# Kernel tuning notes

Hardware: AMD Instinct MI355X
Metric: run time of the kernel (lower is better)

Reference implementation:

```python
import jax, jax.numpy as jnp
import numpy as np

B, T, MAX_ITEMS = 128, 50, 32
NUM_PRODUCT, E, EW = 100000, 128, 16
D = E + EW  # rnn input/hidden size


def setup_inputs() -> dict:
    key = jax.random.key(0)
    ks = jax.random.split(key, 10)
    # items: 0 is padding; keep roughly half the slots padded (ragged baskets)
    items = jax.random.randint(ks[0], (B, T, MAX_ITEMS), 1, NUM_PRODUCT)
    keep = jax.random.uniform(ks[1], (B, T, MAX_ITEMS)) < 0.5
    keep = keep.at[:, :, 0].set(True)  # at least one item per basket
    items = jnp.where(keep, items, 0)
    flag = jax.random.randint(ks[2], (B, T, 1), 0, 2)
    x = jnp.concatenate([items, flag], axis=-1)  # [B,T,MAX_ITEMS+1], last col = flag
    lengths = jnp.full((B,), T, dtype=jnp.int64)
    hidden = jnp.zeros((1, B, D), dtype=jnp.float32)
    s_e = 1.0 / np.sqrt(E)
    s_d = 1.0 / np.sqrt(D)
    encode_w = jax.random.uniform(ks[3], (NUM_PRODUCT, E), minval=-0.1, maxval=0.1)
    encode_w = encode_w.at[0].set(0.0)  # padding_idx=0
    wchange_w = jax.random.normal(ks[4], (2, EW)) * 0.1
    wchange_w = wchange_w.at[0].set(0.0)  # padding_idx=0
    w_ih = jax.random.uniform(ks[5], (3 * D, D), minval=-s_d, maxval=s_d)
    w_hh = jax.random.uniform(ks[6], (3 * D, D), minval=-s_d, maxval=s_d)
    b_ih = jax.random.uniform(ks[7], (3 * D,), minval=-s_d, maxval=s_d)
    b_hh = jax.random.uniform(ks[8], (3 * D,), minval=-s_d, maxval=s_d)
    fc_w = jax.random.uniform(ks[9], (E, D), minval=-s_d, maxval=s_d)
    fc_b = jnp.zeros((E,), dtype=jnp.float32)
    return {"x": x, "lengths": lengths, "hidden": hidden,
            "encode_w": encode_w, "wchange_w": wchange_w,
            "w_ih": w_ih, "w_hh": w_hh, "b_ih": b_ih, "b_hh": b_hh,
            "fc_w": fc_w, "fc_b": fc_b}


def _embed_baskets(x, encode_w, wchange_w):
    items = x[..., :-1]                      # [B,T,I] product ids, 0 = pad
    flag = x[..., -1]                        # [B,T] 0/1 weight-change flag
    emb = encode_w[items]                    # [B,T,I,E] fused ragged gather
    mask = (items != 0).astype(emb.dtype)[..., None]
    cnt = jnp.maximum(mask.sum(axis=2), 1.0)
    pooled = (emb * mask).sum(axis=2) / cnt  # avg pool over real items [B,T,E]
    w = wchange_w[flag]                      # [B,T,EW]
    return jnp.concatenate([pooled, w], axis=-1)  # [B,T,D]


def _gru(seq, h0, w_ih, w_hh, b_ih, b_hh):
    # seq: [B,T,D], h0: [B,D]; torch GRU cell math
    def step(h, x_t):
        gi = x_t @ w_ih.T + b_ih             # [B,3D]
        gh = h @ w_hh.T + b_hh
        i_r, i_z, i_n = jnp.split(gi, 3, axis=-1)
        h_r, h_z, h_n = jnp.split(gh, 3, axis=-1)
        r = jax.nn.sigmoid(i_r + h_r)
        z = jax.nn.sigmoid(i_z + h_z)
        n = jnp.tanh(i_n + r * h_n)
        h_new = (1.0 - z) * n + z * h
        return h_new, h_new
    h_last, outs = jax.lax.scan(step, h0, jnp.swapaxes(seq, 0, 1))
    return jnp.swapaxes(outs, 0, 1), h_last  # [B,T,D], [B,D]


def reference(x, lengths, hidden, encode_w, wchange_w, w_ih, w_hh, b_ih, b_hh, fc_w, fc_b):
    seq = _embed_baskets(x, encode_w, wchange_w)         # [B,T,D]
    out, h_last = _gru(seq, hidden[0], w_ih, w_hh, b_ih, b_hh)
    dynamic_user = out @ fc_w.T + fc_b                   # [B,T,E]
    return dynamic_user, h_last[None]                    # h_u: [1,B,D]
```

## Files before the change

### kernel.cpp

```cpp
#include <hip/hip_runtime.h>
#include <math.h>

#define B_   128
#define T_   50
#define MI_  32
#define E_   128
#define EW_  16
#define D_   144
#define G_   432
#define N_   (B_*T_)

__global__ __launch_bounds__(256) void embed_kernel(
    const int* __restrict__ x,
    const float* __restrict__ encode_w,
    const float* __restrict__ wchange_w,
    float* __restrict__ seq)
{
    int n = blockIdx.x;
    int tid = threadIdx.x;
    int i = tid >> 3;
    int j = tid & 7;

    __shared__ int xi[33];
    __shared__ __align__(16) float part[32 * 132];
    __shared__ float cntf[32];

    if (tid < 33) xi[tid] = x[n * 33 + tid];
    __syncthreads();

    int it = xi[i];
    const float* row = &encode_w[(size_t)it * E_];
    float4 v0 = *(const float4*)&row[16 * j + 0];
    float4 v1 = *(const float4*)&row[16 * j + 4];
    float4 v2 = *(const float4*)&row[16 * j + 8];
    float4 v3 = *(const float4*)&row[16 * j + 12];

    float* p = &part[i * 132 + 16 * j];
    *(float4*)&p[0]  = v0;
    *(float4*)&p[4]  = v1;
    *(float4*)&p[8]  = v2;
    *(float4*)&p[12] = v3;
    if (j == 0) cntf[i] = (it != 0) ? 1.f : 0.f;
    __syncthreads();

    if (tid < E_) {
        int c = tid;
        float s = 0.f, cn = 0.f;
        #pragma unroll
        for (int k = 0; k < 32; ++k) {
            s  += part[k * 132 + c];
            cn += cntf[k];
        }
        seq[n * D_ + c] = s / fmaxf(cn, 1.f);
    } else if (tid < E_ + EW_) {
        int c = tid - E_;
        seq[n * D_ + E_ + c] = wchange_w[xi[32] * EW_ + c];
    }
}

#define GK   144
#define GBK  48
#define GPAD 68

__global__ __launch_bounds__(256) void gemm_bias_kernel(
    const float* __restrict__ A,
    const float* __restrict__ Bw,
    const float* __restrict__ bias,
    float* __restrict__ C,
    int M, int N)
{
    __shared__ float As[GBK * GPAD];
    __shared__ float Bs[GBK * GPAD];

    int tid = threadIdx.x;
    int row0 = blockIdx.x * 64;
    int col0 = blockIdx.y * 64;
    int tx = tid & 15;
    int ty = tid >> 4;

    float acc[4][4] = {};

    int sr = tid >> 2;
    int skq0 = tid & 3;

    for (int k0 = 0; k0 < GK; k0 += GBK) {
        __syncthreads();
        #pragma unroll
        for (int i = 0; i < 3; ++i) {
            int kq = skq0 + i * 4;
            float4 a = *(const float4*)&A[(size_t)(row0 + sr) * GK + k0 + kq * 4];
            int nrow = col0 + sr;
            float4 b = make_float4(0.f, 0.f, 0.f, 0.f);
            if (nrow < N)
                b = *(const float4*)&Bw[(size_t)nrow * GK + k0 + kq * 4];
            As[(kq * 4 + 0) * GPAD + sr] = a.x;
            As[(kq * 4 + 1) * GPAD + sr] = a.y;
            As[(kq * 4 + 2) * GPAD + sr] = a.z;
            As[(kq * 4 + 3) * GPAD + sr] = a.w;
            Bs[(kq * 4 + 0) * GPAD + sr] = b.x;
            Bs[(kq * 4 + 1) * GPAD + sr] = b.y;
            Bs[(kq * 4 + 2) * GPAD + sr] = b.z;
            Bs[(kq * 4 + 3) * GPAD + sr] = b.w;
        }
        __syncthreads();

        #pragma unroll 4
        for (int k = 0; k < GBK; ++k) {
            float4 a4 = *(const float4*)&As[k * GPAD + ty * 4];
            float4 b4 = *(const float4*)&Bs[k * GPAD + tx * 4];
            float av[4] = {a4.x, a4.y, a4.z, a4.w};
            float bv[4] = {b4.x, b4.y, b4.z, b4.w};
            #pragma unroll
            for (int i = 0; i < 4; ++i)
                #pragma unroll
                for (int j = 0; j < 4; ++j)
                    acc[i][j] = fmaf(av[i], bv[j], acc[i][j]);
        }
    }

    int c = col0 + tx * 4;
    if (c < N) {
        float4 bb = *(const float4*)&bias[c];
        #pragma unroll
        for (int i = 0; i < 4; ++i) {
            int r = row0 + ty * 4 + i;
            float4 o;
            o.x = acc[i][0] + bb.x;
            o.y = acc[i][1] + bb.y;
            o.z = acc[i][2] + bb.z;
            o.w = acc[i][3] + bb.w;
            *(float4*)&C[(size_t)r * N + c] = o;
        }
    }
}

template<int CTRL>
__device__ __forceinline__ float dpp_xor_add(float x) {
    int y = __builtin_amdgcn_mov_dpp(__float_as_int(x), CTRL, 0xF, 0xF, true);
    return x + __int_as_float(y);
}

__global__ __launch_bounds__(576) void gru_kernel(
    const float* __restrict__ gi,
    const float* __restrict__ w_hh,
    const float* __restrict__ b_hh,
    const float* __restrict__ h0,
    float* __restrict__ hseq,
    float* __restrict__ hlast)
{
    int b = blockIdx.x;
    int tid = threadIdx.x;
    int g = tid >> 3;
    int s = tid & 7;
    int k0 = s * 20;

    __shared__ __align__(16) float h[160];
    __shared__ float gh[G_];

    float w[6][20];
    #pragma unroll
    for (int r = 0; r < 6; ++r) {
        const float* wrow = &w_hh[(size_t)(6 * g + r) * D_];
        #pragma unroll
        for (int q = 0; q < 5; ++q) {
            int k = k0 + 4 * q;
            float4 t = make_float4(0.f, 0.f, 0.f, 0.f);
            if (k < D_) t = *(const float4*)&wrow[k];
            w[r][4 * q + 0] = t.x;
            w[r][4 * q + 1] = t.y;
            w[r][4 * q + 2] = t.z;
            w[r][4 * q + 3] = t.w;
        }
    }
    float bias = (s < 6) ? b_hh[6 * g + s] : 0.f;

    if (tid < 160) h[tid] = (tid < D_) ? h0[b * D_ + tid] : 0.f;
    __syncthreads();

    for (int t = 0; t < T_; ++t) {
        int n = b * T_ + t;
        float gir = 0.f, giz = 0.f, gin = 0.f;
        if (tid < D_) {
            gir = gi[(size_t)n * G_ + tid];
            giz = gi[(size_t)n * G_ + D_ + tid];
            gin = gi[(size_t)n * G_ + 2 * D_ + tid];
        }

        float hv[20];
        #pragma unroll
        for (int q = 0; q < 5; ++q) {
            float4 t4 = *(const float4*)&h[k0 + 4 * q];
            hv[4 * q + 0] = t4.x;
            hv[4 * q + 1] = t4.y;
            hv[4 * q + 2] = t4.z;
            hv[4 * q + 3] = t4.w;
        }

        float a0 = 0.f, a1 = 0.f, a2 = 0.f, a3 = 0.f, a4 = 0.f, a5 = 0.f;
        #pragma unroll
        for (int kk = 0; kk < 20; ++kk) {
            float hk = hv[kk];
            a0 = fmaf(w[0][kk], hk, a0);
            a1 = fmaf(w[1][kk], hk, a1);
            a2 = fmaf(w[2][kk], hk, a2);
            a3 = fmaf(w[3][kk], hk, a3);
            a4 = fmaf(w[4][kk], hk, a4);
            a5 = fmaf(w[5][kk], hk, a5);
        }

        a0 = dpp_xor_add<0xB1>(a0); a0 = dpp_xor_add<0x4E>(a0); a0 = dpp_xor_add<0x141>(a0);
        a1 = dpp_xor_add<0xB1>(a1); a1 = dpp_xor_add<0x4E>(a1); a1 = dpp_xor_add<0x141>(a1);
        a2 = dpp_xor_add<0xB1>(a2); a2 = dpp_xor_add<0x4E>(a2); a2 = dpp_xor_add<0x141>(a2);
        a3 = dpp_xor_add<0xB1>(a3); a3 = dpp_xor_add<0x4E>(a3); a3 = dpp_xor_add<0x141>(a3);
        a4 = dpp_xor_add<0xB1>(a4); a4 = dpp_xor_add<0x4E>(a4); a4 = dpp_xor_add<0x141>(a4);
        a5 = dpp_xor_add<0xB1>(a5); a5 = dpp_xor_add<0x4E>(a5); a5 = dpp_xor_add<0x141>(a5);

        float myacc = a0;
        if (s == 1) myacc = a1;
        if (s == 2) myacc = a2;
        if (s == 3) myacc = a3;
        if (s == 4) myacc = a4;
        if (s == 5) myacc = a5;
        if (s < 6) gh[6 * g + s] = myacc + bias;
        __syncthreads();

        if (tid < D_) {
            float r = 1.f / (1.f + __expf(-(gir + gh[tid])));
            float z = 1.f / (1.f + __expf(-(giz + gh[D_ + tid])));
            float narg = gin + r * gh[2 * D_ + tid];
            narg = fminf(fmaxf(narg, -15.f), 15.f);
            float e2 = __expf(-2.f * narg);
            float nn = (1.f - e2) / (1.f + e2);
            float hn = (1.f - z) * nn + z * h[tid];
            hseq[(size_t)n * D_ + tid] = hn;
            h[tid] = hn;
        }
        __syncthreads();
    }

    if (tid < D_) hlast[b * D_ + tid] = h[tid];
}

extern "C" void kernel_launch(void* const* d_in, const int* in_sizes, int n_in,
                              void* d_out, int out_size, void* d_ws, size_t ws_size,
                              hipStream_t stream)
{
    const int*   x         = (const int*)d_in[0];
    const float* hidden    = (const float*)d_in[2];
    const float* encode_w  = (const float*)d_in[3];
    const float* wchange_w = (const float*)d_in[4];
    const float* w_ih      = (const float*)d_in[5];
    const float* w_hh      = (const float*)d_in[6];
    const float* b_ih      = (const float*)d_in[7];
    const float* b_hh      = (const float*)d_in[8];
    const float* fc_w      = (const float*)d_in[9];
    const float* fc_b      = (const float*)d_in[10];

    float* out = (float*)d_out;
    float* ws  = (float*)d_ws;
    float* seq  = ws;
    float* gi   = ws + 921600;
    float* hseq = ws + 921600 + 2764800;

    embed_kernel<<<N_, 256, 0, stream>>>(x, encode_w, wchange_w, seq);

    gemm_bias_kernel<<<dim3(N_ / 64, (G_ + 63) / 64), 256, 0, stream>>>(
        seq, w_ih, b_ih, gi, N_, G_);

    gru_kernel<<<B_, 576, 0, stream>>>(gi, w_hh, b_hh, hidden, hseq,
                                       out + (size_t)N_ * E_);

    gemm_bias_kernel<<<dim3(N_ / 64, E_ / 64), 256, 0, stream>>>(
        hseq, fc_w, fc_b, out, N_, E_);
}
```

Before: 186.9 us.

## Fuse embed, input GEMM, GRU and output GEMM into one cooperative kernel

Replaces four kernel launches with a single cooperative kernel of 256 blocks x 512 threads that runs the embedding pool, input projection GEMM, GRU recurrence and FC GEMM as phases separated by grid.sync. The GRU phase now uses 512 threads with 7 weight rows each instead of 576 threads with 6, and buffers the hidden sequence in shared memory before one bulk copy to global. This removes launch gaps and inter-kernel drain, at the cost of grid-wide barriers, fewer blocks (lower parallelism) in the embed and GEMM phases, and more register pressure in the recurrence.

```diff
diff --git a/kernel.cpp b/kernel.cpp
--- a/kernel.cpp
+++ b/kernel.cpp
@@ -1,5 +1,8 @@
 #include <hip/hip_runtime.h>
+#include <hip/hip_cooperative_groups.h>
 #include <math.h>
+
+namespace cg = cooperative_groups;
 
 #define B_   128
 #define T_   50
@@ -10,104 +13,52 @@
 #define G_   432
 #define N_   (B_*T_)
 
-__global__ __launch_bounds__(256) void embed_kernel(
-    const int* __restrict__ x,
-    const float* __restrict__ encode_w,
-    const float* __restrict__ wchange_w,
-    float* __restrict__ seq)
+
+template<int CTRL>
+__device__ __forceinline__ float dpp_xor_add(float x) {
+    int y = __builtin_amdgcn_mov_dpp(__float_as_int(x), CTRL, 0xF, 0xF, true);
+    return x + __int_as_float(y);
+}
+
+__device__ __forceinline__ void gemm_tile_256(
+    int stid, bool valid, int row0, int col0,
+    const float* __restrict__ A, const float* __restrict__ Bw,
+    const float* __restrict__ bias, float* __restrict__ C,
+    int N, float* As, float* Bs)
 {
-    int n = blockIdx.x;
-    int tid = threadIdx.x;
-    int i = tid >> 3;
-    int j = tid & 7;
-
-    __shared__ int xi[33];
-    __shared__ __align__(16) float part[32 * 132];
-    __shared__ float cntf[32];
-
-    if (tid < 33) xi[tid] = x[n * 33 + tid];
-    __syncthreads();
-
-    int it = xi[i];
-    const float* row = &encode_w[(size_t)it * E_];
-    float4 v0 = *(const float4*)&row[16 * j + 0];
-    float4 v1 = *(const float4*)&row[16 * j + 4];
-    float4 v2 = *(const float4*)&row[16 * j + 8];
-    float4 v3 = *(const float4*)&row[16 * j + 12];
-
-    float* p = &part[i * 132 + 16 * j];
-    *(float4*)&p[0]  = v0;
-    *(float4*)&p[4]  = v1;
-    *(float4*)&p[8]  = v2;
-    *(float4*)&p[12] = v3;
-    if (j == 0) cntf[i] = (it != 0) ? 1.f : 0.f;
-    __syncthreads();
-
-    if (tid < E_) {
-        int c = tid;
-        float s = 0.f, cn = 0.f;
-        #pragma unroll
-        for (int k = 0; k < 32; ++k) {
-            s  += part[k * 132 + c];
-            cn += cntf[k];
-        }
-        seq[n * D_ + c] = s / fmaxf(cn, 1.f);
-    } else if (tid < E_ + EW_) {
-        int c = tid - E_;
-        seq[n * D_ + E_ + c] = wchange_w[xi[32] * EW_ + c];
-    }
-}
-
-#define GK   144
-#define GBK  48
-#define GPAD 68
-
-__global__ __launch_bounds__(256) void gemm_bias_kernel(
-    const float* __restrict__ A,
-    const float* __restrict__ Bw,
-    const float* __restrict__ bias,
-    float* __restrict__ C,
-    int M, int N)
-{
-    __shared__ float As[GBK * GPAD];
-    __shared__ float Bs[GBK * GPAD];
-
-    int tid = threadIdx.x;
-    int row0 = blockIdx.x * 64;
-    int col0 = blockIdx.y * 64;
-    int tx = tid & 15;
-    int ty = tid >> 4;
-
+    int tx = stid & 15;
+    int ty = stid >> 4;
     float acc[4][4] = {};
-
-    int sr = tid >> 2;
-    int skq0 = tid & 3;
-
-    for (int k0 = 0; k0 < GK; k0 += GBK) {
+    int sr = stid >> 2;
+    int skq0 = stid & 3;
+
+    for (int k0 = 0; k0 < 144; k0 += 48) {
         __syncthreads();
         #pragma unroll
         for (int i = 0; i < 3; ++i) {
             int kq = skq0 + i * 4;
-            float4 a = *(const float4*)&A[(size_t)(row0 + sr) * GK + k0 + kq * 4];
+            float4 a = make_float4(0.f, 0.f, 0.f, 0.f);
+            float4 b = make_float4(0.f, 0.f, 0.f, 0.f);
+            if (valid)
+                a = *(const float4*)&A[(size_t)(row0 + sr) * 144 + k0 + kq * 4];
             int nrow = col0 + sr;
-            float4 b = make_float4(0.f, 0.f, 0.f, 0.f);
-            if (nrow < N)
-                b = *(const float4*)&Bw[(size_t)nrow * GK + k0 + kq * 4];
-            As[(kq * 4 + 0) * GPAD + sr] = a.x;
-            As[(kq * 4 + 1) * GPAD + sr] = a.y;
-            As[(kq * 4 + 2) * GPAD + sr] = a.z;
-            As[(kq * 4 + 3) * GPAD + sr] = a.w;
-            Bs[(kq * 4 + 0) * GPAD + sr] = b.x;
-            Bs[(kq * 4 + 1) * GPAD + sr] = b.y;
-            Bs[(kq * 4 + 2) * GPAD + sr] = b.z;
-            Bs[(kq * 4 + 3) * GPAD + sr] = b.w;
+            if (valid && nrow < N)
+                b = *(const float4*)&Bw[(size_t)nrow * 144 + k0 + kq * 4];
+            As[(kq * 4 + 0) * 68 + sr] = a.x;
+            As[(kq * 4 + 1) * 68 + sr] = a.y;
+            As[(kq * 4 + 2) * 68 + sr] = a.z;
+            As[(kq * 4 + 3) * 68 + sr] = a.w;
+            Bs[(kq * 4 + 0) * 68 + sr] = b.x;
+            Bs[(kq * 4 + 1) * 68 + sr] = b.y;
+            Bs[(kq * 4 + 2) * 68 + sr] = b.z;
+            Bs[(kq * 4 + 3) * 68 + sr] = b.w;
         }
         __syncthreads();
 
         #pragma unroll 4
-        for (int k = 0; k < GBK; ++k) {
-            float4 a4 = *(const float4*)&As[k * GPAD + ty * 4];
-            float4 b4 = *(const float4*)&Bs[k * GPAD + tx * 4];
+        for (int k = 0; k < 48; ++k) {
+            float4 a4 = *(const float4*)&As[k * 68 + ty * 4];
+            float4 b4 = *(const float4*)&Bs[k * 68 + tx * 4];
             float av[4] = {a4.x, a4.y, a4.z, a4.w};
             float bv[4] = {b4.x, b4.y, b4.z, b4.w};
             #pragma unroll
@@ -119,7 +70,7 @@
     }
 
     int c = col0 + tx * 4;
-    if (c < N) {
+    if (valid && c < N) {
         float4 bb = *(const float4*)&bias[c];
         #pragma unroll
         for (int i = 0; i < 4; ++i) {
@@ -134,111 +85,210 @@
     }
 }
 
-template<int CTRL>
-__device__ __forceinline__ float dpp_xor_add(float x) {
-    int y = __builtin_amdgcn_mov_dpp(__float_as_int(x), CTRL, 0xF, 0xF, true);
-    return x + __int_as_float(y);
-}
-
-__global__ __launch_bounds__(576) void gru_kernel(
-    const float* __restrict__ gi,
+__global__ __launch_bounds__(512, 2) void mega_kernel(
+    const int*   __restrict__ x,
+    const float* __restrict__ hidden,
+    const float* __restrict__ encode_w,
+    const float* __restrict__ wchange_w,
+    const float* __restrict__ w_ih,
     const float* __restrict__ w_hh,
+    const float* __restrict__ b_ih,
     const float* __restrict__ b_hh,
-    const float* __restrict__ h0,
-    float* __restrict__ hseq,
-    float* __restrict__ hlast)
+    const float* __restrict__ fc_w,
+    const float* __restrict__ fc_b,
+    float* __restrict__ out,
+    float* __restrict__ seq,
+    float* __restrict__ gi,
+    float* __restrict__ hseq)
 {
-    int b = blockIdx.x;
+    cg::grid_group grid = cg::this_grid();
+
+    __shared__ __align__(16) float smem[13056];
+
+    int bid = blockIdx.x;
     int tid = threadIdx.x;
-    int g = tid >> 3;
-    int s = tid & 7;
-    int k0 = s * 20;
-
-    __shared__ __align__(16) float h[160];
-    __shared__ float gh[G_];
-
-    float w[6][20];
-    #pragma unroll
-    for (int r = 0; r < 6; ++r) {
-        const float* wrow = &w_hh[(size_t)(6 * g + r) * D_];
+    int sub = tid >> 8;
+    int stid = tid & 255;
+
+    {
+        float* eb   = smem + sub * 4352;
+        int*   xi   = (int*)eb;
+        float* part = eb + 48;
+        float* cntf = eb + 48 + 4224;
+        int i = stid >> 3;
+        int j = stid & 7;
+
+        for (int r = 0; r < 13; ++r) {
+            int n = r * 512 + 2 * bid + sub;
+            bool v = (n < N_);
+            if (v && stid < 33) xi[stid] = x[n * 33 + stid];
+            __syncthreads();
+
+            if (v) {
+                int it = xi[i];
+                const float* row = &encode_w[(size_t)it * E_];
+                float4 v0 = *(const float4*)&row[16 * j + 0];
+                float4 v1 = *(const float4*)&row[16 * j + 4];
+                float4 v2 = *(const float4*)&row[16 * j + 8];
+                float4 v3 = *(const float4*)&row[16 * j + 12];
+                float* p = &part[i * 132 + 16 * j];
+                *(float4*)&p[0]  = v0;
+                *(float4*)&p[4]  = v1;
+                *(float4*)&p[8]  = v2;
+                *(float4*)&p[12] = v3;
+                if (j == 0) cntf[i] = (it != 0) ? 1.f : 0.f;
+            }
+            __syncthreads();
+
+            if (v && stid < E_) {
+                float s = 0.f, cn = 0.f;
+                #pragma unroll
+                for (int k = 0; k < 32; ++k) {
+                    s  += part[k * 132 + stid];
+                    cn += cntf[k];
+                }
+                seq[n * D_ + stid] = s / fmaxf(cn, 1.f);
+            } else if (v && stid < E_ + EW_) {
+                int c = stid - E_;
+                seq[n * D_ + E_ + c] = wchange_w[xi[32] * EW_ + c];
+            }
+            __syncthreads();
+        }
+    }
+    grid.sync();
+
+    {
+        float* gb = smem + sub * 6528;
+        float* As = gb;
+        float* Bs = gb + 3264;
+        for (int r = 0; r < 2; ++r) {
+            int t = r * 512 + 2 * bid + sub;
+            bool valid = (t < 700);
+            int tt = valid ? t : 0;
+            int row0 = (tt / 7) * 64;
+            int col0 = (tt % 7) * 64;
+            gemm_tile_256(stid, valid, row0, col0, seq, w_ih, b_ih, gi, G_, As, Bs);
+        }
+    }
+    grid.sync();
+
+    if (bid < B_) {
+        int b = bid;
+        int g = tid >> 3;
+        int s = tid & 7;
+        int k0 = s * 20;
+
+        float* h    = smem;
+        float* gh   = smem + 160;
+        float* hbuf = smem + 592;
+
+        float w[7][20];
         #pragma unroll
-        for (int q = 0; q < 5; ++q) {
-            int k = k0 + 4 * q;
-            float4 t = make_float4(0.f, 0.f, 0.f, 0.f);
-            if (k < D_) t = *(const float4*)&wrow[k];
-            w[r][4 * q + 0] = t.x;
-            w[r][4 * q + 1] = t.y;
-            w[r][4 * q + 2] = t.z;
-            w[r][4 * q + 3] = t.w;
-        }
-    }
-    float bias = (s < 6) ? b_hh[6 * g + s] : 0.f;
-
-    if (tid < 160) h[tid] = (tid < D_) ? h0[b * D_ + tid] : 0.f;
-    __syncthreads();
-
-    for (int t = 0; t < T_; ++t) {
-        int n = b * T_ + t;
-        float gir = 0.f, giz = 0.f, gin = 0.f;
-        if (tid < D_) {
-            gir = gi[(size_t)n * G_ + tid];
-            giz = gi[(size_t)n * G_ + D_ + tid];
-            gin = gi[(size_t)n * G_ + 2 * D_ + tid];
-        }
-
-        float hv[20];
-        #pragma unroll
-        for (int q = 0; q < 5; ++q) {
-            float4 t4 = *(const float4*)&h[k0 + 4 * q];
-            hv[4 * q + 0] = t4.x;
-            hv[4 * q + 1] = t4.y;
-            hv[4 * q + 2] = t4.z;
-            hv[4 * q + 3] = t4.w;
-        }
-
-        float a0 = 0.f, a1 = 0.f, a2 = 0.f, a3 = 0.f, a4 = 0.f, a5 = 0.f;
-        #pragma unroll
-        for (int kk = 0; kk < 20; ++kk) {
-            float hk = hv[kk];
-            a0 = fmaf(w[0][kk], hk, a0);
-            a1 = fmaf(w[1][kk], hk, a1);
-            a2 = fmaf(w[2][kk], hk, a2);
-            a3 = fmaf(w[3][kk], hk, a3);
-            a4 = fmaf(w[4][kk], hk, a4);
-            a5 = fmaf(w[5][kk], hk, a5);
-        }
-
-        a0 = dpp_xor_add<0xB1>(a0); a0 = dpp_xor_add<0x4E>(a0); a0 = dpp_xor_add<0x141>(a0);
-        a1 = dpp_xor_add<0xB1>(a1); a1 = dpp_xor_add<0x4E>(a1); a1 = dpp_xor_add<0x141>(a1);
-        a2 = dpp_xor_add<0xB1>(a2); a2 = dpp_xor_add<0x4E>(a2); a2 = dpp_xor_add<0x141>(a2);
-        a3 = dpp_xor_add<0xB1>(a3); a3 = dpp_xor_add<0x4E>(a3); a3 = dpp_xor_add<0x141>(a3);
-        a4 = dpp_xor_add<0xB1>(a4); a4 = dpp_xor_add<0x4E>(a4); a4 = dpp_xor_add<0x141>(a4);
-        a5 = dpp_xor_add<0xB1>(a5); a5 = dpp_xor_add<0x4E>(a5); a5 = dpp_xor_add<0x141>(a5);
-
-        float myacc = a0;
-        if (s == 1) myacc = a1;
-        if (s == 2) myacc = a2;
-        if (s == 3) myacc = a3;
-        if (s == 4) myacc = a4;
-        if (s == 5) myacc = a5;
-        if (s < 6) gh[6 * g + s] = myacc + bias;
+        for (int rr = 0; rr < 7; ++rr) {
+            int row = 7 * g + rr;
+            if (row > 431) row = 431;
+            const float* wrow = &w_hh[(size_t)row * D_];
+            #pragma unroll
+            for (int q = 0; q < 5; ++q) {
+                int k = k0 + 4 * q;
+                float4 t4 = make_float4(0.f, 0.f, 0.f, 0.f);
+                if (k < D_) t4 = *(const float4*)&wrow[k];
+                w[rr][4 * q + 0] = t4.x;
+                w[rr][4 * q + 1] = t4.y;
+                w[rr][4 * q + 2] = t4.z;
+                w[rr][4 * q + 3] = t4.w;
+            }
+        }
+        int myrow = 7 * g + s;
+        float bias = b_hh[(myrow > 431) ? 431 : myrow];
+
+        if (tid < 160) h[tid] = (tid < D_) ? hidden[b * D_ + tid] : 0.f;
         __syncthreads();
 
-        if (tid < D_) {
-            float r = 1.f / (1.f + __expf(-(gir + gh[tid])));
-            float z = 1.f / (1.f + __expf(-(giz + gh[D_ + tid])));
-            float narg = gin + r * gh[2 * D_ + tid];
-            narg = fminf(fmaxf(narg, -15.f), 15.f);
-            float e2 = __expf(-2.f * narg);
-            float nn = (1.f - e2) / (1.f + e2);
-            float hn = (1.f - z) * nn + z * h[tid];
-            hseq[(size_t)n * D_ + tid] = hn;
-            h[tid] = hn;
-        }
-        __syncthreads();
-    }
-
-    if (tid < D_) hlast[b * D_ + tid] = h[tid];
+        for (int t = 0; t < T_; ++t) {
+            int n = b * T_ + t;
+            float gir = 0.f, giz = 0.f, gin = 0.f;
+            if (tid < D_) {
+                gir = gi[(size_t)n * G_ + tid];
+                giz = gi[(size_t)n * G_ + D_ + tid];
+                gin = gi[(size_t)n * G_ + 2 * D_ + tid];
+            }
+
+            float hv[20];
+            #pragma unroll
+            for (int q = 0; q < 5; ++q) {
+                float4 t4 = *(const float4*)&h[k0 + 4 * q];
+                hv[4 * q + 0] = t4.x;
+                hv[4 * q + 1] = t4.y;
+                hv[4 * q + 2] = t4.z;
+                hv[4 * q + 3] = t4.w;
+            }
+
+            float a0 = 0.f, a1 = 0.f, a2 = 0.f, a3 = 0.f, a4 = 0.f, a5 = 0.f, a6 = 0.f;
+            #pragma unroll
+            for (int kk = 0; kk < 20; ++kk) {
+                float hk = hv[kk];
+                a0 = fmaf(w[0][kk], hk, a0);
+                a1 = fmaf(w[1][kk], hk, a1);
+                a2 = fmaf(w[2][kk], hk, a2);
+                a3 = fmaf(w[3][kk], hk, a3);
+                a4 = fmaf(w[4][kk], hk, a4);
+                a5 = fmaf(w[5][kk], hk, a5);
+                a6 = fmaf(w[6][kk], hk, a6);
+            }
+
+            a0 = dpp_xor_add<0xB1>(a0); a0 = dpp_xor_add<0x4E>(a0); a0 = dpp_xor_add<0x141>(a0);
+            a1 = dpp_xor_add<0xB1>(a1); a1 = dpp_xor_add<0x4E>(a1); a1 = dpp_xor_add<0x141>(a1);
+            a2 = dpp_xor_add<0xB1>(a2); a2 = dpp_xor_add<0x4E>(a2); a2 = dpp_xor_add<0x141>(a2);
+            a3 = dpp_xor_add<0xB1>(a3); a3 = dpp_xor_add<0x4E>(a3); a3 = dpp_xor_add<0x141>(a3);
+            a4 = dpp_xor_add<0xB1>(a4); a4 = dpp_xor_add<0x4E>(a4); a4 = dpp_xor_add<0x141>(a4);
+            a5 = dpp_xor_add<0xB1>(a5); a5 = dpp_xor_add<0x4E>(a5); a5 = dpp_xor_add<0x141>(a5);
+            a6 = dpp_xor_add<0xB1>(a6); a6 = dpp_xor_add<0x4E>(a6); a6 = dpp_xor_add<0x141>(a6);
+
+            float myacc = a0;
+            if (s == 1) myacc = a1;
+            if (s == 2) myacc = a2;
+            if (s == 3) myacc = a3;
+            if (s == 4) myacc = a4;
+            if (s == 5) myacc = a5;
+            if (s == 6) myacc = a6;
+            if (s < 7 && myrow < G_) gh[myrow] = myacc + bias;
+            __syncthreads();
+
+            if (tid < D_) {
+                float r = 1.f / (1.f + __expf(-(gir + gh[tid])));
+                float z = 1.f / (1.f + __expf(-(giz + gh[D_ + tid])));
+                float narg = gin + r * gh[2 * D_ + tid];
+                narg = fminf(fmaxf(narg, -15.f), 15.f);
+                float e2 = __expf(-2.f * narg);
+                float nn = (1.f - e2) / (1.f + e2);
+                float hn = (1.f - z) * nn + z * h[tid];
+                hbuf[t * D_ + tid] = hn;
+                h[tid] = hn;
+            }
+            __syncthreads();
+        }
+
+        {
+            const float4* src = (const float4*)hbuf;
+            float4* dst = (float4*)&hseq[(size_t)b * T_ * D_];
+            for (int i2 = tid; i2 < (T_ * D_) / 4; i2 += 512) dst[i2] = src[i2];
+        }
+        if (tid < D_) out[(size_t)N_ * E_ + b * D_ + tid] = h[tid];
+    }
+    grid.sync();
+
+    {
+        float* gb = smem + sub * 6528;
+        float* As = gb;
+        float* Bs = gb + 3264;
+        int t = 2 * bid + sub;
+        bool valid = (t < 200);
+        int tt = valid ? t : 0;
+        int row0 = (tt >> 1) * 64;
+        int col0 = (tt & 1) * 64;
+        gemm_tile_256(stid, valid, row0, col0, hseq, fc_w, fc_b, out, E_, As, Bs);
+    }
 }
 
 extern "C" void kernel_launch(void* const* d_in, const int* in_sizes, int n_in,
@@ -256,20 +306,18 @@
     const float* fc_w      = (const float*)d_in[9];
     const float* fc_b      = (const float*)d_in[10];
 
-    float* out = (float*)d_out;
-    float* ws  = (float*)d_ws;
+    float* out  = (float*)d_out;
+    float* ws   = (float*)d_ws;
     float* seq  = ws;
     float* gi   = ws + 921600;
     float* hseq = ws + 921600 + 2764800;
 
-    embed_kernel<<<N_, 256, 0, stream>>>(x, encode_w, wchange_w, seq);
-
-    gemm_bias_kernel<<<dim3(N_ / 64, (G_ + 63) / 64), 256, 0, stream>>>(
-        seq, w_ih, b_ih, gi, N_, G_);
-
-    gru_kernel<<<B_, 576, 0, stream>>>(gi, w_hh, b_hh, hidden, hseq,
-                                       out + (size_t)N_ * E_);
-
-    gemm_bias_kernel<<<dim3(N_ / 64, E_ / 64), 256, 0, stream>>>(
-        hseq, fc_w, fc_b, out, N_, E_);
+    void* args[] = {
+        (void*)&x, (void*)&hidden, (void*)&encode_w, (void*)&wchange_w,
+        (void*)&w_ih, (void*)&w_hh, (void*)&b_ih, (void*)&b_hh,
+        (void*)&fc_w, (void*)&fc_b,
+        (void*)&out, (void*)&seq, (void*)&gi, (void*)&hseq
+    };
+    hipLaunchCooperativeKernel((void*)mega_kernel, dim3(256), dim3(512),
+                               args, 0, stream);
 }
```

Result: slower. 318.3 us (+70.3%).

## Batch 16 sequences per GRU block and compute recurrent matmul with bf16 MFMA

Applied to the files above, without the earlier changes.

The GRU recurrence now runs 16 batch rows per workgroup (8 blocks instead of 128) and computes h@W_hh^T with 16x16x32 bf16 MFMA instructions. W_hh is held in registers as bf16 fragments, and h is split into hi/lo bf16 parts to keep near-fp32 accuracy. The aim is to replace per-thread scalar FMA dot products and DPP reductions with matrix-core throughput, amortising the weight registers over many sequences. The cost is far fewer blocks, so most CUs sit idle during the serial 50-step loop, plus bf16 rounding of the weights.

```diff
diff --git a/kernel.cpp b/kernel.cpp
--- a/kernel.cpp
+++ b/kernel.cpp
@@ -9,6 +9,18 @@
 #define D_   144
 #define G_   432
 #define N_   (B_*T_)
+
+typedef short bf16x8 __attribute__((ext_vector_type(8)));
+typedef float f32x4  __attribute__((ext_vector_type(4)));
+
+__device__ __forceinline__ short f2bf(float f) {
+    unsigned u = __float_as_uint(f);
+    u = (u + 0x7FFFu + ((u >> 16) & 1u)) >> 16;
+    return (short)u;
+}
+__device__ __forceinline__ float bf2f(short s) {
+    return __uint_as_float(((unsigned)(unsigned short)s) << 16);
+}
 
 __global__ __launch_bounds__(256) void embed_kernel(
     const int* __restrict__ x,
@@ -134,13 +146,7 @@
     }
 }
 
-template<int CTRL>
-__device__ __forceinline__ float dpp_xor_add(float x) {
-    int y = __builtin_amdgcn_mov_dpp(__float_as_int(x), CTRL, 0xF, 0xF, true);
-    return x + __int_as_float(y);
-}
-
-__global__ __launch_bounds__(576) void gru_kernel(
+__global__ __launch_bounds__(512, 1) void gru_kernel(
     const float* __restrict__ gi,
     const float* __restrict__ w_hh,
     const float* __restrict__ b_hh,
@@ -148,97 +154,152 @@
     float* __restrict__ hseq,
     float* __restrict__ hlast)
 {
-    int b = blockIdx.x;
-    int tid = threadIdx.x;
-    int g = tid >> 3;
-    int s = tid & 7;
-    int k0 = s * 20;
-
-    __shared__ __align__(16) float h[160];
-    __shared__ float gh[G_];
-
-    float w[6][20];
+    int bb   = blockIdx.x;
+    int tid  = threadIdx.x;
+    int wave = tid >> 6;
+    int lane = tid & 63;
+    int ln   = lane & 15;
+    int qd   = lane >> 4;
+
+    __shared__ short hH[16 * 168];
+    __shared__ short hL[16 * 168];
+    __shared__ float gh[16 * 434];
+
+    bf16x8 wf[4][5];
     #pragma unroll
-    for (int r = 0; r < 6; ++r) {
-        const float* wrow = &w_hh[(size_t)(6 * g + r) * D_];
-        #pragma unroll
-        for (int q = 0; q < 5; ++q) {
-            int k = k0 + 4 * q;
-            float4 t = make_float4(0.f, 0.f, 0.f, 0.f);
-            if (k < D_) t = *(const float4*)&wrow[k];
-            w[r][4 * q + 0] = t.x;
-            w[r][4 * q + 1] = t.y;
-            w[r][4 * q + 2] = t.z;
-            w[r][4 * q + 3] = t.w;
-        }
-    }
-    float bias = (s < 6) ? b_hh[6 * g + s] : 0.f;
-
-    if (tid < 160) h[tid] = (tid < D_) ? h0[b * D_ + tid] : 0.f;
+    for (int ti = 0; ti < 4; ++ti) {
+        int tn = wave + 8 * ti;
+        bool tvalid = (tn < 27);
+        int tnc = tvalid ? tn : 0;
+        const float* wr = &w_hh[(size_t)(tnc * 16 + ln) * 144];
+        #pragma unroll
+        for (int kt = 0; kt < 5; ++kt) {
+            bool kval = tvalid && ((kt < 4) || (qd < 2));
+            int kb = kt * 32 + qd * 8;
+            float4 f0 = make_float4(0.f, 0.f, 0.f, 0.f);
+            float4 f1 = make_float4(0.f, 0.f, 0.f, 0.f);
+            if (kval) {
+                f0 = *(const float4*)&wr[kb];
+                f1 = *(const float4*)&wr[kb + 4];
+            }
+            bf16x8 v;
+            v[0] = f2bf(f0.x); v[1] = f2bf(f0.y); v[2] = f2bf(f0.z); v[3] = f2bf(f0.w);
+            v[4] = f2bf(f1.x); v[5] = f2bf(f1.y); v[6] = f2bf(f1.z); v[7] = f2bf(f1.w);
+            wf[ti][kt] = v;
+        }
+    }
+
+    int m = tid >> 5;
+    int dbase = tid & 31;
+    int bglob = bb * 16 + m;
+
+    float bhr[5], bhz[5], bhn[5], hold[5], hnreg[5];
+    #pragma unroll
+    for (int it = 0; it < 5; ++it) {
+        int d = dbase + 32 * it;
+        bool v = d < D_;
+        bhr[it]   = v ? b_hh[d]        : 0.f;
+        bhz[it]   = v ? b_hh[D_ + d]   : 0.f;
+        bhn[it]   = v ? b_hh[2*D_ + d] : 0.f;
+        hold[it]  = v ? h0[bglob * D_ + d] : 0.f;
+        hnreg[it] = 0.f;
+    }
+
+    for (int i = tid; i < 16 * 168; i += 512) { hH[i] = 0; hL[i] = 0; }
     __syncthreads();
-
-    for (int t = 0; t < T_; ++t) {
-        int n = b * T_ + t;
-        float gir = 0.f, giz = 0.f, gin = 0.f;
-        if (tid < D_) {
-            gir = gi[(size_t)n * G_ + tid];
-            giz = gi[(size_t)n * G_ + D_ + tid];
-            gin = gi[(size_t)n * G_ + 2 * D_ + tid];
-        }
-
-        float hv[20];
-        #pragma unroll
-        for (int q = 0; q < 5; ++q) {
-            float4 t4 = *(const float4*)&h[k0 + 4 * q];
-            hv[4 * q + 0] = t4.x;
-            hv[4 * q + 1] = t4.y;
-            hv[4 * q + 2] = t4.z;
-            hv[4 * q + 3] = t4.w;
-        }
-
-        float a0 = 0.f, a1 = 0.f, a2 = 0.f, a3 = 0.f, a4 = 0.f, a5 = 0.f;
-        #pragma unroll
-        for (int kk = 0; kk < 20; ++kk) {
-            float hk = hv[kk];
-            a0 = fmaf(w[0][kk], hk, a0);
-            a1 = fmaf(w[1][kk], hk, a1);
-            a2 = fmaf(w[2][kk], hk, a2);
-            a3 = fmaf(w[3][kk], hk, a3);
-            a4 = fmaf(w[4][kk], hk, a4);
-            a5 = fmaf(w[5][kk], hk, a5);
-        }
-
-        a0 = dpp_xor_add<0xB1>(a0); a0 = dpp_xor_add<0x4E>(a0); a0 = dpp_xor_add<0x141>(a0);
-        a1 = dpp_xor_add<0xB1>(a1); a1 = dpp_xor_add<0x4E>(a1); a1 = dpp_xor_add<0x141>(a1);
-        a2 = dpp_xor_add<0xB1>(a2); a2 = dpp_xor_add<0x4E>(a2); a2 = dpp_xor_add<0x141>(a2);
-        a3 = dpp_xor_add<0xB1>(a3); a3 = dpp_xor_add<0x4E>(a3); a3 = dpp_xor_add<0x141>(a3);
-        a4 = dpp_xor_add<0xB1>(a4); a4 = dpp_xor_add<0x4E>(a4); a4 = dpp_xor_add<0x141>(a4);
-        a5 = dpp_xor_add<0xB1>(a5); a5 = dpp_xor_add<0x4E>(a5); a5 = dpp_xor_add<0x141>(a5);
-
-        float myacc = a0;
-        if (s == 1) myacc = a1;
-        if (s == 2) myacc = a2;
-        if (s == 3) myacc = a3;
-        if (s == 4) myacc = a4;
-        if (s == 5) myacc = a5;
-        if (s < 6) gh[6 * g + s] = myacc + bias;
+    #pragma unroll
+    for (int it = 0; it < 5; ++it) {
+        int d = dbase + 32 * it;
+        if (d < D_) {
+            short hi = f2bf(hold[it]);
+            hH[m * 168 + d] = hi;
+            hL[m * 168 + d] = f2bf(hold[it] - bf2f(hi));
+        }
+    }
+    __syncthreads();
+
+    const float* gib = &gi[(size_t)bglob * T_ * G_];
+
+    for (int step = 0; step < T_; ++step) {
+        if (step > 0) {
+            float* hs = &hseq[((size_t)bglob * T_ + (step - 1)) * D_];
+            #pragma unroll
+            for (int it = 0; it < 5; ++it) {
+                int d = dbase + 32 * it;
+                if (d < D_) hs[d] = hnreg[it];
+            }
+        }
+        const float* gp = &gib[(size_t)step * G_];
+        float gir[5], giz[5], gin[5];
+        #pragma unroll
+        for (int it = 0; it < 5; ++it) {
+            int d = dbase + 32 * it;
+            bool v = d < D_;
+            gir[it] = v ? gp[d]        : 0.f;
+            giz[it] = v ? gp[D_ + d]   : 0.f;
+            gin[it] = v ? gp[2*D_ + d] : 0.f;
+        }
+
+        bf16x8 ah[5], al[5];
+        #pragma unroll
+        for (int kt = 0; kt < 5; ++kt) {
+            ah[kt] = *(bf16x8*)&hH[ln * 168 + kt * 32 + qd * 8];
+            al[kt] = *(bf16x8*)&hL[ln * 168 + kt * 32 + qd * 8];
+        }
+
+        #pragma unroll
+        for (int ti = 0; ti < 4; ++ti) {
+            int tn = wave + 8 * ti;
+            if (tn < 27) {
+                f32x4 acc = {0.f, 0.f, 0.f, 0.f};
+                #pragma unroll
+                for (int kt = 0; kt < 5; ++kt) {
+                    acc = __builtin_amdgcn_mfma_f32_16x16x32_bf16(ah[kt], wf[ti][kt], acc, 0, 0, 0);
+                    acc = __builtin_amdgcn_mfma_f32_16x16x32_bf16(al[kt], wf[ti][kt], acc, 0, 0, 0);
+                }
+                int n = tn * 16 + ln;
+                #pragma unroll
+                for (int i = 0; i < 4; ++i)
+                    gh[(qd * 4 + i) * 434 + n] = acc[i];
+            }
+        }
         __syncthreads();
 
-        if (tid < D_) {
-            float r = 1.f / (1.f + __expf(-(gir + gh[tid])));
-            float z = 1.f / (1.f + __expf(-(giz + gh[D_ + tid])));
-            float narg = gin + r * gh[2 * D_ + tid];
-            narg = fminf(fmaxf(narg, -15.f), 15.f);
-            float e2 = __expf(-2.f * narg);
-            float nn = (1.f - e2) / (1.f + e2);
-            float hn = (1.f - z) * nn + z * h[tid];
-            hseq[(size_t)n * D_ + tid] = hn;
-            h[tid] = hn;
+        #pragma unroll
+        for (int it = 0; it < 5; ++it) {
+            int d = dbase + 32 * it;
+            if (d < D_) {
+                float ghr = gh[m * 434 + d];
+                float ghz = gh[m * 434 + D_ + d];
+                float ghn = gh[m * 434 + 2*D_ + d];
+                float r = 1.f / (1.f + __expf(-(gir[it] + ghr + bhr[it])));
+                float z = 1.f / (1.f + __expf(-(giz[it] + ghz + bhz[it])));
+                float narg = gin[it] + r * (ghn + bhn[it]);
+                narg = fminf(fmaxf(narg, -15.f), 15.f);
+                float e2 = __expf(-2.f * narg);
+                float nn = (1.f - e2) / (1.f + e2);
+                float hn = (1.f - z) * nn + z * hold[it];
+                hold[it] = hn;
+                hnreg[it] = hn;
+                short hi = f2bf(hn);
+                hH[m * 168 + d] = hi;
+                hL[m * 168 + d] = f2bf(hn - bf2f(hi));
+            }
         }
         __syncthreads();
     }
 
-    if (tid < D_) hlast[b * D_ + tid] = h[tid];
+    {
+        float* hs = &hseq[((size_t)bglob * T_ + (T_ - 1)) * D_];
+        #pragma unroll
+        for (int it = 0; it < 5; ++it) {
+            int d = dbase + 32 * it;
+            if (d < D_) {
+                hs[d] = hnreg[it];
+                hlast[bglob * D_ + d] = hold[it];
+            }
+        }
+    }
 }
 
 extern "C" void kernel_launch(void* const* d_in, const int* in_sizes, int n_in,
@@ -267,8 +328,8 @@
     gemm_bias_kernel<<<dim3(N_ / 64, (G_ + 63) / 64), 256, 0, stream>>>(
         seq, w_ih, b_ih, gi, N_, G_);
 
-    gru_kernel<<<B_, 576, 0, stream>>>(gi, w_hh, b_hh, hidden, hseq,
-                                       out + (size_t)N_ * E_);
+    gru_kernel<<<8, 512, 0, stream>>>(gi, w_hh, b_hh, hidden, hseq,
+                                      out + (size_t)N_ * E_);
 
     gemm_bias_kernel<<<dim3(N_ / 64, E_ / 64), 256, 0, stream>>>(
         hseq, fc_w, fc_b, out, N_, E_);
```

New measurement: 252.5 us. 1.35x slower.
